# Kernel tuning notes

Measured on AMD Instinct MI355X. Metric: run time of the kernel, lower is better.

## Reference

```python
import jax, jax.numpy as jnp
import numpy as np

B, L, SD, PD, H, HD, OH = 2, 256, 64, 32, 4, 16, 32
EXP = 64  # MBConv hidden = pair_dim * expand_ratio(2)
SE = 16   # squeezed channels = int(64 * 0.25)


def _ln(x, g, b, eps=1e-5):
    m = jnp.mean(x, -1, keepdims=True)
    v = jnp.mean((x - m) ** 2, -1, keepdims=True)
    return (x - m) / jnp.sqrt(v + eps) * g + b


def _inorm(x, eps=1e-5):  # InstanceNorm2d (no affine), x: [B,C,H,W]
    m = jnp.mean(x, (2, 3), keepdims=True)
    v = jnp.mean((x - m) ** 2, (2, 3), keepdims=True)
    return (x - m) / jnp.sqrt(v + eps)


def setup_inputs() -> dict:
    key = jax.random.key(0)
    ks = jax.random.split(key, 16)
    s = jnp.float32(0.02)
    return dict(
        seq_repr=jax.random.normal(ks[0], (B, L, SD), jnp.float32),
        pair_repr=jax.random.normal(ks[1], (B, L, L, PD), jnp.float32),
        g_attn=jnp.ones((SD,), jnp.float32), b_attn=jnp.zeros((SD,), jnp.float32),
        g_pair=jnp.ones((PD,), jnp.float32), b_pair=jnp.zeros((PD,), jnp.float32),
        W_opm_lin=jax.random.normal(ks[2], (SD, OH), jnp.float32) * s,
        b_opm_lin=jnp.zeros((OH,), jnp.float32),
        g_opm=jnp.ones((OH * OH,), jnp.float32), b_opm=jnp.zeros((OH * OH,), jnp.float32),
        W_opm_proj=jax.random.normal(ks[3], (OH * OH, PD), jnp.float32) * s,
        b_opm_proj=jnp.zeros((PD,), jnp.float32),
        W_exp=jax.random.normal(ks[4], (EXP, PD), jnp.float32) * s,
        W_dw=jax.random.normal(ks[5], (EXP, 1, 3, 3), jnp.float32) * s,
        W_se1=jax.random.normal(ks[6], (SE, EXP), jnp.float32) * s,
        b_se1=jnp.zeros((SE,), jnp.float32),
        W_se2=jax.random.normal(ks[7], (EXP, SE), jnp.float32) * s,
        b_se2=jnp.zeros((EXP,), jnp.float32),
        W_pw=jax.random.normal(ks[8], (PD, EXP), jnp.float32) * s,
        W_qkv=jax.random.normal(ks[9], (SD, 3 * SD), jnp.float32) * s,
        W_outp=jax.random.normal(ks[10], (SD, SD), jnp.float32) * s,
        b_outp=jnp.zeros((SD,), jnp.float32),
        W_bias=jax.random.normal(ks[11], (PD, H), jnp.float32) * s,
    )


def reference(seq_repr, pair_repr, g_attn, b_attn, g_pair, b_pair,
              W_opm_lin, b_opm_lin, g_opm, b_opm, W_opm_proj, b_opm_proj,
              W_exp, W_dw, W_se1, b_se1, W_se2, b_se2, W_pw,
              W_qkv, W_outp, b_outp, W_bias):
    # --- OuterProductMean on attn_norm(seq) ---
    x = _ln(seq_repr, g_attn, b_attn)                            # [B,L,SD]
    a = x @ W_opm_lin + b_opm_lin                                # [B,L,OH]
    outer = jnp.einsum('bid,bje->bijde', a, a).reshape(B, L, L, OH * OH)
    op = _ln(outer, g_opm, b_opm) @ W_opm_proj + b_opm_proj      # [B,L,L,PD]
    pair = pair_repr + op
    # --- MBConv pair processor on pair_norm(pair) ---
    pn = _ln(pair, g_pair, b_pair)
    z0 = jnp.transpose(pn, (0, 3, 1, 2))                         # NCHW [B,PD,L,L]
    h = jax.nn.silu(_inorm(jnp.einsum('bcij,oc->boij', z0, W_exp)))
    h = jax.lax.conv_general_dilated(h, W_dw, (1, 1), 'SAME',
                                     feature_group_count=EXP,
                                     dimension_numbers=('NCHW', 'OIHW', 'NCHW'))
    h = jax.nn.silu(_inorm(h))
    sq = jnp.mean(h, (2, 3), keepdims=True)                      # squeeze [B,EXP,1,1]
    sq = jax.nn.silu(jnp.einsum('bcij,oc->boij', sq, W_se1) + b_se1[None, :, None, None])
    sq = jax.nn.sigmoid(jnp.einsum('bcij,oc->boij', sq, W_se2) + b_se2[None, :, None, None])
    h = h * sq
    h = _inorm(jnp.einsum('bcij,oc->boij', h, W_pw))             # project back to PD
    pair = pair + jnp.transpose(z0 + h, (0, 2, 3, 1))            # MBConv residual + outer residual
    # --- Pairwise-bias attention ---
    pn2 = _ln(pair, g_pair, b_pair)
    bias = jnp.einsum('bijp,ph->bhij', pn2, W_bias)              # [B,H,L,L]
    q, k, v = jnp.split(x @ W_qkv, 3, axis=-1)
    q = q.reshape(B, L, H, HD).transpose(0, 2, 1, 3)
    k = k.reshape(B, L, H, HD).transpose(0, 2, 1, 3)
    v = v.reshape(B, L, H, HD).transpose(0, 2, 1, 3)
    scores = jnp.einsum('bhid,bhjd->bhij', q, k) / jnp.sqrt(jnp.float32(HD)) + bias
    w = jax.nn.softmax(scores, axis=-1)
    ctx = jnp.einsum('bhij,bhjd->bhid', w, v).transpose(0, 2, 1, 3).reshape(B, L, SD)
    seq = seq_repr + ctx @ W_outp + b_outp
    return seq, pair
```

## Files before the change

### kernel.cpp

```cpp
#include <hip/hip_runtime.h>
#include <hip/hip_bf16.h>

#define LLSZ 65536
#define INV_LL (1.f / 65536.f)


__global__ __launch_bounds__(1024) void k0_prep(
    const float* __restrict__ g_opm, const float* __restrict__ b_opm,
    const float* __restrict__ Wproj, const float* __restrict__ b_proj,
    float* __restrict__ G, float* __restrict__ GW, float* __restrict__ BW)
{
    int tid = threadIdx.x;
    int p = tid & 31, rg = tid >> 5;
    float gw = 0.f, bw = 0.f;
    #pragma unroll 4
    for (int k = 0; k < 32; ++k) {
        int de = k * 32 + rg;
        float g = g_opm[de], b = b_opm[de];
        float wv = Wproj[de * 32 + p];
        float gv = g * wv;
        G[de * 32 + p] = gv;
        gw += gv;
        bw += b * wv;
    }
    __shared__ float rG[1024], rB[1024];
    rG[rg * 32 + p] = gw;
    rB[rg * 32 + p] = bw;
    __syncthreads();
    for (int s = 16; s > 0; s >>= 1) {
        if (rg < s) {
            rG[rg * 32 + p] += rG[(rg + s) * 32 + p];
            rB[rg * 32 + p] += rB[(rg + s) * 32 + p];
        }
        __syncthreads();
    }
    if (tid < 32) {
        GW[p] = rG[p];
        BW[p] = rB[p] + b_proj[p];
    }
}

__global__ __launch_bounds__(256) void k1_seq(
    const float* __restrict__ seq, const float* __restrict__ g_attn,
    const float* __restrict__ b_attn, const float* __restrict__ W_lin,
    const float* __restrict__ b_lin, const float* __restrict__ W_qkv,
    float* __restrict__ a, float* __restrict__ am, float* __restrict__ s2,
    float* __restrict__ qkv)
{
    __shared__ float Wq[64 * 192];
    __shared__ float Wl[64 * 32];
    __shared__ float xL[4][64];
    int tid = threadIdx.x;
    #pragma unroll
    for (int k = 0; k < 48; ++k) Wq[k * 256 + tid] = W_qkv[k * 256 + tid];
    #pragma unroll
    for (int k = 0; k < 8; ++k) Wl[k * 256 + tid] = W_lin[k * 256 + tid];

    int sub = tid >> 6, t = tid & 63;
    int row = blockIdx.x * 4 + sub;
    float v = seq[row * 64 + t];
    float m = v;
    for (int k = 32; k > 0; k >>= 1) m += __shfl_xor(m, k, 64);
    m *= (1.f / 64.f);
    float d = v - m;
    float var = d * d;
    for (int k = 32; k > 0; k >>= 1) var += __shfl_xor(var, k, 64);
    var *= (1.f / 64.f);
    float x = d * rsqrtf(var + 1e-5f) * g_attn[t] + b_attn[t];
    xL[sub][t] = x;
    __syncthreads();

    if (t < 32) {
        float s = 0.f;
        #pragma unroll
        for (int dd = 0; dd < 64; ++dd) s += xL[sub][dd] * Wl[dd * 32 + t];
        s += b_lin[t];
        a[row * 32 + t] = s;
        float mm = s, ss = s * s;
        for (int k = 16; k > 0; k >>= 1) {
            mm += __shfl_xor(mm, k, 32);
            ss += __shfl_xor(ss, k, 32);
        }
        if (t == 0) { am[row] = mm * (1.f / 32.f); s2[row] = ss * (1.f / 32.f); }
    }
    #pragma unroll
    for (int c3 = 0; c3 < 3; ++c3) {
        int c = c3 * 64 + t;
        float s = 0.f;
        #pragma unroll
        for (int dd = 0; dd < 64; ++dd) s += xL[sub][dd] * Wq[dd * 192 + c];
        qkv[row * 192 + c] = s;
    }
}

__global__ __launch_bounds__(256) void k2_T(
    const float* __restrict__ a, const float* __restrict__ G, float* __restrict__ T)
{
    int row = blockIdx.x;
    int tid = threadIdx.x;
    __shared__ float aL[32];
    if (tid < 32) aL[tid] = a[row * 32 + tid];
    __syncthreads();
    for (int k = 0; k < 4; ++k) {
        int idx = k * 256 + tid;
        float s = 0.f;
        #pragma unroll
        for (int d = 0; d < 32; ++d) s += aL[d] * G[d * 1024 + idx];
        T[row * 1024 + idx] = s;
    }
}

__global__ __launch_bounds__(256) void k3_op(
    const float* __restrict__ a, const float* __restrict__ am,
    const float* __restrict__ s2, const float* __restrict__ T,
    const float* __restrict__ GW, const float* __restrict__ BW,
    const float* __restrict__ pair_in, const float* __restrict__ g_pair,
    const float* __restrict__ b_pair, float* __restrict__ pair1,
    float* __restrict__ pn)
{
    int row = blockIdx.x;
    int b = row >> 8;
    int tid = threadIdx.x;
    __shared__ float Tl[1024];
    __shared__ float aL[256];
    for (int k = 0; k < 4; ++k) Tl[k * 256 + tid] = T[(long)row * 1024 + k * 256 + tid];
    float am_i = am[row], s2_i = s2[row];
    int jj = tid >> 5, p = tid & 31;
    float gw = GW[p], bw = BW[p], gp = g_pair[p], bp = b_pair[p];
    for (int jt = 0; jt < 32; ++jt) {
        __syncthreads();
        aL[tid] = a[(b * 256 + jt * 8) * 32 + tid];
        __syncthreads();
        int j = jt * 8 + jj;
        float am_j = am[b * 256 + j], s2_j = s2[b * 256 + j];
        float S = 0.f;
        #pragma unroll
        for (int e = 0; e < 32; ++e) S += aL[jj * 32 + e] * Tl[e * 32 + p];
        float m = am_i * am_j;
        float var = s2_i * s2_j - m * m;
        float isd = rsqrtf(var + 1e-5f);
        float op = isd * (S - m * gw) + bw;
        long idx = (long)row * 8192 + jt * 256 + tid;
        float pv = pair_in[idx] + op;
        pair1[idx] = pv;
        float mu = pv;
        for (int k = 16; k > 0; k >>= 1) mu += __shfl_xor(mu, k, 32);
        mu *= (1.f / 32.f);
        float dd = pv - mu;
        float vv = dd * dd;
        for (int k = 16; k > 0; k >>= 1) vv += __shfl_xor(vv, k, 32);
        vv *= (1.f / 32.f);
        pn[idx] = dd * rsqrtf(vv + 1e-5f) * gp + bp;
    }
}

__global__ __launch_bounds__(256) void k4_expand(
    const float* __restrict__ pn, const float* __restrict__ W_exp,
    float* __restrict__ e1)
{
    int blk = blockIdx.x;
    int b = blk >> 8;
    int pixbase = (blk & 255) * 256;
    int tid = threadIdx.x;
    __shared__ float pnL[256 * 33];
    __shared__ float We[64 * 32];
    for (int k = 0; k < 32; ++k) {
        int idx = k * 256 + tid;
        float v = pn[(long)b * LLSZ * 32 + (long)pixbase * 32 + idx];
        int pix = idx >> 5, c = idx & 31;
        pnL[pix * 33 + c] = v;
    }
    for (int k = 0; k < 8; ++k) We[k * 256 + tid] = W_exp[k * 256 + tid];
    __syncthreads();
    for (int o = 0; o < 64; ++o) {
        float s = 0.f;
        #pragma unroll
        for (int c = 0; c < 32; ++c) s += pnL[tid * 33 + c] * We[o * 32 + c];
        e1[(long)(b * 64 + o) * LLSZ + pixbase + tid] = s;
    }
}

__global__ __launch_bounds__(256) void k_stats(
    const float* __restrict__ buf, float* __restrict__ sum, float* __restrict__ sumsq)
{
    int bid = blockIdx.x;
    int chan = bid >> 3, seg = bid & 7;
    int tid = threadIdx.x;
    const float4* p = (const float4*)(buf + (long)chan * LLSZ + seg * 8192);
    float s = 0.f, ss = 0.f;
    #pragma unroll
    for (int k = 0; k < 8; ++k) {
        float4 v = p[k * 256 + tid];
        s += v.x + v.y + v.z + v.w;
        ss += v.x * v.x + v.y * v.y + v.z * v.z + v.w * v.w;
    }
    for (int k = 32; k > 0; k >>= 1) { s += __shfl_xor(s, k, 64); ss += __shfl_xor(ss, k, 64); }
    __shared__ float rs[4], rq[4];
    int wave = tid >> 6;
    if ((tid & 63) == 0) { rs[wave] = s; rq[wave] = ss; }
    __syncthreads();
    if (tid == 0) {
        atomicAdd(&sum[chan], rs[0] + rs[1] + rs[2] + rs[3]);
        atomicAdd(&sumsq[chan], rq[0] + rq[1] + rq[2] + rq[3]);
    }
}

__device__ __forceinline__ void chan_stats(const float* sum, const float* sumsq,
                                           int chan, float& m, float& isd)
{
    m = sum[chan] * INV_LL;
    float var = sumsq[chan] * INV_LL - m * m;
    isd = rsqrtf(var + 1e-5f);
}

__global__ __launch_bounds__(256) void k6_dw(
    const float* __restrict__ e1, const float* __restrict__ st1s,
    const float* __restrict__ st1q, const float* __restrict__ W_dw,
    float* __restrict__ h2)
{
    int blk = blockIdx.x;
    int chan = blk >> 6;
    int tile = blk & 63;
    int i0 = (tile >> 3) * 32, j0 = (tile & 7) * 32;
    int o = chan & 63;
    int tid = threadIdx.x;
    float m, isd;
    chan_stats(st1s, st1q, chan, m, isd);
    __shared__ float hT[34 * 34];
    const float* src = e1 + (long)chan * LLSZ;
    for (int idx = tid; idx < 1156; idx += 256) {
        int li = idx / 34, lj = idx % 34;
        int gi = i0 + li - 1, gj = j0 + lj - 1;
        float v = 0.f;
        if (gi >= 0 && gi < 256 && gj >= 0 && gj < 256) {
            float t = (src[gi * 256 + gj] - m) * isd;
            v = t / (1.f + expf(-t));
        }
        hT[idx] = v;
    }
    float w[9];
    #pragma unroll
    for (int k = 0; k < 9; ++k) w[k] = W_dw[o * 9 + k];
    __syncthreads();
    for (int q = 0; q < 4; ++q) {
        int pix = q * 256 + tid;
        int li = pix >> 5, lj = pix & 31;
        float s = 0.f;
        #pragma unroll
        for (int ki = 0; ki < 3; ++ki)
            #pragma unroll
            for (int kj = 0; kj < 3; ++kj)
                s += hT[(li + ki) * 34 + lj + kj] * w[ki * 3 + kj];
        h2[(long)chan * LLSZ + (i0 + li) * 256 + j0 + lj] = s;
    }
}

__global__ __launch_bounds__(256) void k8_squeeze(
    const float* __restrict__ h2, const float* __restrict__ st2s,
    const float* __restrict__ st2q, float* __restrict__ sqs)
{
    int bid = blockIdx.x;
    int chan = bid >> 3, seg = bid & 7;
    int tid = threadIdx.x;
    float m, isd;
    chan_stats(st2s, st2q, chan, m, isd);
    const float4* p = (const float4*)(h2 + (long)chan * LLSZ + seg * 8192);
    float s = 0.f;
    #pragma unroll
    for (int k = 0; k < 8; ++k) {
        float4 v = p[k * 256 + tid];
        float t;
        t = (v.x - m) * isd; s += t / (1.f + expf(-t));
        t = (v.y - m) * isd; s += t / (1.f + expf(-t));
        t = (v.z - m) * isd; s += t / (1.f + expf(-t));
        t = (v.w - m) * isd; s += t / (1.f + expf(-t));
    }
    for (int k = 32; k > 0; k >>= 1) s += __shfl_xor(s, k, 64);
    __shared__ float rs[4];
    int wave = tid >> 6;
    if ((tid & 63) == 0) rs[wave] = s;
    __syncthreads();
    if (tid == 0) atomicAdd(&sqs[chan], rs[0] + rs[1] + rs[2] + rs[3]);
}

__global__ __launch_bounds__(128) void k9_se(
    const float* __restrict__ sqs, const float* __restrict__ W1,
    const float* __restrict__ b1, const float* __restrict__ W2,
    const float* __restrict__ b2, float* __restrict__ sqv)
{
    __shared__ float s1[2 * 16];
    int tid = threadIdx.x;
    if (tid < 32) {
        int b = tid >> 4, o = tid & 15;
        float s = 0.f;
        for (int c = 0; c < 64; ++c) s += sqs[b * 64 + c] * W1[o * 64 + c];
        s = s * INV_LL + b1[o];
        s1[b * 16 + o] = s / (1.f + expf(-s));
    }
    __syncthreads();
    int b = tid >> 6, c = tid & 63;
    float s = 0.f;
    #pragma unroll
    for (int j = 0; j < 16; ++j) s += s1[b * 16 + j] * W2[c * 16 + j];
    s += b2[c];
    sqv[b * 64 + c] = 1.f / (1.f + expf(-s));
}

__global__ __launch_bounds__(256) void k10_pw(
    const float* __restrict__ h2, const float* __restrict__ st2s,
    const float* __restrict__ st2q, const float* __restrict__ sqv,
    const float* __restrict__ W_pw, float* __restrict__ hp)
{
    int blk = blockIdx.x;
    int b = blk >> 8;
    int pixbase = (blk & 255) * 256;
    int tid = threadIdx.x;
    __shared__ float hL[32 * 256];
    __shared__ float Wp[32 * 64];
    for (int k = 0; k < 8; ++k) Wp[k * 256 + tid] = W_pw[k * 256 + tid];
    float acc[32];
    #pragma unroll
    for (int p = 0; p < 32; ++p) acc[p] = 0.f;
    for (int half = 0; half < 2; ++half) {
        __syncthreads();
        for (int c = 0; c < 32; ++c) {
            int chan = b * 64 + half * 32 + c;
            float m, isd;
            chan_stats(st2s, st2q, chan, m, isd);
            float v = h2[(long)chan * LLSZ + pixbase + tid];
            float t = (v - m) * isd;
            hL[c * 256 + tid] = (t / (1.f + expf(-t))) * sqv[chan];
        }
        __syncthreads();
        #pragma unroll
        for (int p = 0; p < 32; ++p) {
            float s = 0.f;
            #pragma unroll
            for (int c = 0; c < 32; ++c) s += hL[c * 256 + tid] * Wp[p * 64 + half * 32 + c];
            acc[p] += s;
        }
    }
    for (int p = 0; p < 32; ++p)
        hp[(long)(b * 32 + p) * LLSZ + pixbase + tid] = acc[p];
}

__global__ __launch_bounds__(256) void k12_merge(
    const float* __restrict__ pair1, const float* __restrict__ pn,
    const float* __restrict__ hp, const float* __restrict__ st3s,
    const float* __restrict__ st3q, const float* __restrict__ g_pair,
    const float* __restrict__ b_pair, const float* __restrict__ W_bias,
    float* __restrict__ pair_out, float* __restrict__ biasbuf)
{
    int blk = blockIdx.x;
    int b = blk >> 8;
    int pixbase = (blk & 255) * 256;
    int tid = threadIdx.x;
    __shared__ float hpL[32 * 257];
    for (int p = 0; p < 32; ++p) {
        int chan = b * 32 + p;
        float m, isd;
        chan_stats(st3s, st3q, chan, m, isd);
        float v = hp[(long)chan * LLSZ + pixbase + tid];
        hpL[p * 257 + tid] = (v - m) * isd;
    }
    __syncthreads();
    int jj = tid >> 5, p = tid & 31;
    float gp = g_pair[p], bp = b_pair[p];
    float wb0 = W_bias[p * 4 + 0], wb1 = W_bias[p * 4 + 1];
    float wb2 = W_bias[p * 4 + 2], wb3 = W_bias[p * 4 + 3];
    for (int it = 0; it < 32; ++it) {
        int pix = it * 8 + jj;
        long idx = (long)b * LLSZ * 32 + (long)(pixbase + pix) * 32 + p;
        float v = pair1[idx] + pn[idx] + hpL[p * 257 + pix];
        pair_out[idx] = v;
        float mu = v;
        for (int k = 16; k > 0; k >>= 1) mu += __shfl_xor(mu, k, 32);
        mu *= (1.f / 32.f);
        float d = v - mu;
        float vv = d * d;
        for (int k = 16; k > 0; k >>= 1) vv += __shfl_xor(vv, k, 32);
        vv *= (1.f / 32.f);
        float pn2 = d * rsqrtf(vv + 1e-5f) * gp + bp;
        float t0 = pn2 * wb0, t1 = pn2 * wb1, t2 = pn2 * wb2, t3 = pn2 * wb3;
        for (int k = 16; k > 0; k >>= 1) {
            t0 += __shfl_xor(t0, k, 32);
            t1 += __shfl_xor(t1, k, 32);
            t2 += __shfl_xor(t2, k, 32);
            t3 += __shfl_xor(t3, k, 32);
        }
        if (p == 0) {
            int ij = pixbase + pix;
            biasbuf[(long)(b * 4 + 0) * LLSZ + ij] = t0;
            biasbuf[(long)(b * 4 + 1) * LLSZ + ij] = t1;
            biasbuf[(long)(b * 4 + 2) * LLSZ + ij] = t2;
            biasbuf[(long)(b * 4 + 3) * LLSZ + ij] = t3;
        }
    }
}

__global__ __launch_bounds__(256) void k13_attn(
    const float* __restrict__ qkv, const float* __restrict__ biasbuf,
    float* __restrict__ ctx)
{
    int blk = blockIdx.x;
    int i = blk & 255;
    int h = (blk >> 8) & 3;
    int b = blk >> 10;
    int tid = threadIdx.x;
    __shared__ float qL[16];
    __shared__ float red[256];
    __shared__ float wL[256];
    __shared__ float pL[256];
    if (tid < 16) qL[tid] = qkv[(long)(b * 256 + i) * 192 + h * 16 + tid];
    __syncthreads();
    const float* krow = qkv + (long)(b * 256 + tid) * 192 + 64 + h * 16;
    float s = 0.f;
    #pragma unroll
    for (int d = 0; d < 16; ++d) s += qL[d] * krow[d];
    s = s * 0.25f + biasbuf[(long)(b * 4 + h) * LLSZ + i * 256 + tid];
    red[tid] = s;
    __syncthreads();
    for (int k = 128; k > 0; k >>= 1) {
        if (tid < k) red[tid] = fmaxf(red[tid], red[tid + k]);
        __syncthreads();
    }
    float mx = red[0];
    __syncthreads();
    float w = expf(s - mx);
    wL[tid] = w;
    red[tid] = w;
    __syncthreads();
    for (int k = 128; k > 0; k >>= 1) {
        if (tid < k) red[tid] += red[tid + k];
        __syncthreads();
    }
    float inv = 1.f / red[0];
    int d = tid & 15, jg = tid >> 4;
    const float* vbase = qkv + 128 + h * 16 + d;
    float ps = 0.f;
    #pragma unroll
    for (int jjj = 0; jjj < 16; ++jjj) {
        int jn = jg * 16 + jjj;
        ps += wL[jn] * vbase[(long)(b * 256 + jn) * 192];
    }
    pL[tid] = ps;
    __syncthreads();
    if (tid < 16) {
        float c = 0.f;
        #pragma unroll
        for (int jg2 = 0; jg2 < 16; ++jg2) c += pL[jg2 * 16 + tid];
        ctx[(long)(b * 256 + i) * 64 + h * 16 + tid] = c * inv;
    }
}

__global__ __launch_bounds__(256) void k14_seqout(
    const float* __restrict__ seq, const float* __restrict__ ctx,
    const float* __restrict__ W_outp, const float* __restrict__ b_outp,
    float* __restrict__ out)
{
    __shared__ float Wo[64 * 64];
    __shared__ float cL[4][64];
    int tid = threadIdx.x;
    #pragma unroll
    for (int k = 0; k < 16; ++k) Wo[k * 256 + tid] = W_outp[k * 256 + tid];
    int sub = tid >> 6, t = tid & 63;
    int row = blockIdx.x * 4 + sub;
    cL[sub][t] = ctx[row * 64 + t];
    __syncthreads();
    float s = b_outp[t];
    #pragma unroll
    for (int u = 0; u < 64; ++u) s += cL[sub][u] * Wo[u * 64 + t];
    out[row * 64 + t] = seq[row * 64 + t] + s;
}

extern "C" void kernel_launch(void* const* d_in, const int* in_sizes, int n_in,
                              void* d_out, int out_size, void* d_ws, size_t ws_size,
                              hipStream_t stream) {
    const float* seq_repr   = (const float*)d_in[0];
    const float* pair_repr  = (const float*)d_in[1];
    const float* g_attn     = (const float*)d_in[2];
    const float* b_attn     = (const float*)d_in[3];
    const float* g_pair     = (const float*)d_in[4];
    const float* b_pair     = (const float*)d_in[5];
    const float* W_opm_lin  = (const float*)d_in[6];
    const float* b_opm_lin  = (const float*)d_in[7];
    const float* g_opm      = (const float*)d_in[8];
    const float* b_opm      = (const float*)d_in[9];
    const float* W_opm_proj = (const float*)d_in[10];
    const float* b_opm_proj = (const float*)d_in[11];
    const float* W_exp      = (const float*)d_in[12];
    const float* W_dw       = (const float*)d_in[13];
    const float* W_se1      = (const float*)d_in[14];
    const float* b_se1      = (const float*)d_in[15];
    const float* W_se2      = (const float*)d_in[16];
    const float* b_se2      = (const float*)d_in[17];
    const float* W_pw       = (const float*)d_in[18];
    const float* W_qkv      = (const float*)d_in[19];
    const float* W_outp     = (const float*)d_in[20];
    const float* b_outp     = (const float*)d_in[21];
    const float* W_bias     = (const float*)d_in[22];

    float* out_seq  = (float*)d_out;
    float* out_pair = (float*)d_out + 32768;

    float* w = (float*)d_ws;
    float* a_buf   = w;
    float* am_buf  = a_buf + 16384;
    float* s2_buf  = am_buf + 512;
    float* qkv_buf = s2_buf + 512;
    float* G_buf   = qkv_buf + 98304;
    float* GW_buf  = G_buf + 32768;
    float* BW_buf  = GW_buf + 32;
    float* ctx     = BW_buf + 32;
    float* st1s    = ctx + 32768;
    float* st1q    = st1s + 128;
    float* st2s    = st1q + 128;
    float* st2q    = st2s + 128;
    float* st3s    = st2q + 128;
    float* st3q    = st3s + 64;
    float* sqs     = st3q + 64;
    float* sqv     = sqs + 128;
    float* T_buf   = sqv + 128;
    float* biasb   = T_buf;
    float* pair1   = T_buf + 524288;
    float* pn      = pair1 + 4194304;
    float* e1      = pn + 4194304;
    float* hp      = e1;
    float* h2      = e1 + 8388608;

    hipMemsetAsync(st1s, 0, 768 * sizeof(float), stream);

    hipLaunchKernelGGL(k0_prep, dim3(1), dim3(1024), 0, stream,
                       g_opm, b_opm, W_opm_proj, b_opm_proj, G_buf, GW_buf, BW_buf);
    hipLaunchKernelGGL(k1_seq, dim3(128), dim3(256), 0, stream,
                       seq_repr, g_attn, b_attn, W_opm_lin, b_opm_lin, W_qkv,
                       a_buf, am_buf, s2_buf, qkv_buf);
    hipLaunchKernelGGL(k2_T, dim3(512), dim3(256), 0, stream, a_buf, G_buf, T_buf);
    hipLaunchKernelGGL(k3_op, dim3(512), dim3(256), 0, stream,
                       a_buf, am_buf, s2_buf, T_buf, GW_buf, BW_buf,
                       pair_repr, g_pair, b_pair, pair1, pn);
    hipLaunchKernelGGL(k4_expand, dim3(512), dim3(256), 0, stream, pn, W_exp, e1);
    hipLaunchKernelGGL(k_stats, dim3(1024), dim3(256), 0, stream, e1, st1s, st1q);
    hipLaunchKernelGGL(k6_dw, dim3(8192), dim3(256), 0, stream, e1, st1s, st1q, W_dw, h2);
    hipLaunchKernelGGL(k_stats, dim3(1024), dim3(256), 0, stream, h2, st2s, st2q);
    hipLaunchKernelGGL(k8_squeeze, dim3(1024), dim3(256), 0, stream, h2, st2s, st2q, sqs);
    hipLaunchKernelGGL(k9_se, dim3(1), dim3(128), 0, stream,
                       sqs, W_se1, b_se1, W_se2, b_se2, sqv);
    hipLaunchKernelGGL(k10_pw, dim3(512), dim3(256), 0, stream,
                       h2, st2s, st2q, sqv, W_pw, hp);
    hipLaunchKernelGGL(k_stats, dim3(512), dim3(256), 0, stream, hp, st3s, st3q);
    hipLaunchKernelGGL(k12_merge, dim3(512), dim3(256), 0, stream,
                       pair1, pn, hp, st3s, st3q, g_pair, b_pair, W_bias,
                       out_pair, biasb);
    hipLaunchKernelGGL(k13_attn, dim3(2048), dim3(256), 0, stream, qkv_buf, biasb, ctx);
    hipLaunchKernelGGL(k14_seqout, dim3(128), dim3(256), 0, stream,
                       seq_repr, ctx, W_outp, b_outp, out_seq);
}
```

Measured before the change: 329.2 us.

## Fuse LayerNorm recompute, SE and stats into neighbors; vectorize and retile kernels

```diff
diff --git a/kernel.cpp b/kernel.cpp
--- a/kernel.cpp
+++ b/kernel.cpp
@@ -4,6 +4,16 @@
 #define LLSZ 65536
 #define INV_LL (1.f / 65536.f)
 
+
+__device__ __forceinline__ void chan_stats(const float* sum, const float* sumsq,
+                                           int chan, float& m, float& isd)
+{
+    m = sum[chan] * INV_LL;
+    float var = sumsq[chan] * INV_LL - m * m;
+    isd = rsqrtf(var + 1e-5f);
+}
+
+__device__ __forceinline__ float silu(float t) { return t / (1.f + expf(-t)); }
 
 __global__ __launch_bounds__(1024) void k0_prep(
     const float* __restrict__ g_opm, const float* __restrict__ b_opm,
@@ -16,12 +26,11 @@
     #pragma unroll 4
     for (int k = 0; k < 32; ++k) {
         int de = k * 32 + rg;
-        float g = g_opm[de], b = b_opm[de];
         float wv = Wproj[de * 32 + p];
-        float gv = g * wv;
+        float gv = g_opm[de] * wv;
         G[de * 32 + p] = gv;
         gw += gv;
-        bw += b * wv;
+        bw += b_opm[de] * wv;
     }
     __shared__ float rG[1024], rB[1024];
     rG[rg * 32 + p] = gw;
@@ -34,10 +43,7 @@
         }
         __syncthreads();
     }
-    if (tid < 32) {
-        GW[p] = rG[p];
-        BW[p] = rB[p] + b_proj[p];
-    }
+    if (tid < 32) { GW[p] = rG[p]; BW[p] = rB[p] + b_proj[p]; }
 }
 
 __global__ __launch_bounds__(256) void k1_seq(
@@ -114,69 +120,88 @@
     const float* __restrict__ a, const float* __restrict__ am,
     const float* __restrict__ s2, const float* __restrict__ T,
     const float* __restrict__ GW, const float* __restrict__ BW,
-    const float* __restrict__ pair_in, const float* __restrict__ g_pair,
-    const float* __restrict__ b_pair, float* __restrict__ pair1,
-    float* __restrict__ pn)
-{
-    int row = blockIdx.x;
+    const float* __restrict__ pair_in, float* __restrict__ pair1)
+{
+    int blk = blockIdx.x;
+    int row = blk >> 3;
+    int jg = blk & 7;
     int b = row >> 8;
+    int j0 = jg * 32;
     int tid = threadIdx.x;
     __shared__ float Tl[1024];
-    __shared__ float aL[256];
-    for (int k = 0; k < 4; ++k) Tl[k * 256 + tid] = T[(long)row * 1024 + k * 256 + tid];
+    __shared__ float aL[32 * 33];
+    __shared__ float amL[32], s2L[32], gwL[32], bwL[32];
+    ((float4*)Tl)[tid] = ((const float4*)(T + (long)row * 1024))[tid];
+    for (int k = 0; k < 4; ++k) {
+        int idx = k * 256 + tid;
+        aL[(idx >> 5) * 33 + (idx & 31)] = a[(b * 256 + j0) * 32 + idx];
+    }
+    if (tid < 32) {
+        amL[tid] = am[b * 256 + j0 + tid];
+        s2L[tid] = s2[b * 256 + j0 + tid];
+        gwL[tid] = GW[tid];
+        bwL[tid] = BW[tid];
+    }
+    __syncthreads();
+    int jl = tid >> 3, cq = tid & 7;
     float am_i = am[row], s2_i = s2[row];
-    int jj = tid >> 5, p = tid & 31;
-    float gw = GW[p], bw = BW[p], gp = g_pair[p], bp = b_pair[p];
-    for (int jt = 0; jt < 32; ++jt) {
-        __syncthreads();
-        aL[tid] = a[(b * 256 + jt * 8) * 32 + tid];
-        __syncthreads();
-        int j = jt * 8 + jj;
-        float am_j = am[b * 256 + j], s2_j = s2[b * 256 + j];
+    float m = am_i * amL[jl];
+    float isd = rsqrtf(s2_i * s2L[jl] - m * m + 1e-5f);
+    long base = ((long)row * 256 + j0 + jl) * 32 + cq * 4;
+    float4 pv = *(const float4*)(pair_in + base);
+    float o[4];
+    #pragma unroll
+    for (int u = 0; u < 4; ++u) {
+        int p = cq * 4 + u;
         float S = 0.f;
         #pragma unroll
-        for (int e = 0; e < 32; ++e) S += aL[jj * 32 + e] * Tl[e * 32 + p];
-        float m = am_i * am_j;
-        float var = s2_i * s2_j - m * m;
-        float isd = rsqrtf(var + 1e-5f);
-        float op = isd * (S - m * gw) + bw;
-        long idx = (long)row * 8192 + jt * 256 + tid;
-        float pv = pair_in[idx] + op;
-        pair1[idx] = pv;
-        float mu = pv;
-        for (int k = 16; k > 0; k >>= 1) mu += __shfl_xor(mu, k, 32);
-        mu *= (1.f / 32.f);
-        float dd = pv - mu;
-        float vv = dd * dd;
-        for (int k = 16; k > 0; k >>= 1) vv += __shfl_xor(vv, k, 32);
-        vv *= (1.f / 32.f);
-        pn[idx] = dd * rsqrtf(vv + 1e-5f) * gp + bp;
-    }
+        for (int e = 0; e < 32; ++e) S += aL[jl * 33 + e] * Tl[e * 32 + p];
+        o[u] = isd * (S - m * gwL[p]) + bwL[p];
+    }
+    pv.x += o[0]; pv.y += o[1]; pv.z += o[2]; pv.w += o[3];
+    *(float4*)(pair1 + base) = pv;
 }
 
 __global__ __launch_bounds__(256) void k4_expand(
-    const float* __restrict__ pn, const float* __restrict__ W_exp,
+    const float* __restrict__ pair1, const float* __restrict__ g_pair,
+    const float* __restrict__ b_pair, const float* __restrict__ W_exp,
     float* __restrict__ e1)
 {
     int blk = blockIdx.x;
-    int b = blk >> 8;
-    int pixbase = (blk & 255) * 256;
-    int tid = threadIdx.x;
-    __shared__ float pnL[256 * 33];
-    __shared__ float We[64 * 32];
-    for (int k = 0; k < 32; ++k) {
+    int b = blk >> 9;
+    int pixbase = (blk & 511) * 128;
+    int tid = threadIdx.x;
+    __shared__ float pnL[128 * 33];
+    __shared__ float We[2048];
+    __shared__ float gL[32], bL[32];
+    for (int k = 0; k < 8; ++k) We[k * 256 + tid] = W_exp[k * 256 + tid];
+    if (tid < 32) { gL[tid] = g_pair[tid]; bL[tid] = b_pair[tid]; }
+    const float4* src = (const float4*)(pair1 + ((long)b * LLSZ + pixbase) * 32);
+    for (int k = 0; k < 4; ++k) {
         int idx = k * 256 + tid;
-        float v = pn[(long)b * LLSZ * 32 + (long)pixbase * 32 + idx];
-        int pix = idx >> 5, c = idx & 31;
-        pnL[pix * 33 + c] = v;
-    }
-    for (int k = 0; k < 8; ++k) We[k * 256 + tid] = W_exp[k * 256 + tid];
-    __syncthreads();
-    for (int o = 0; o < 64; ++o) {
-        float s = 0.f;
-        #pragma unroll
-        for (int c = 0; c < 32; ++c) s += pnL[tid * 33 + c] * We[o * 32 + c];
-        e1[(long)(b * 64 + o) * LLSZ + pixbase + tid] = s;
+        int pix = idx >> 3, cq = idx & 7;
+        float4 v = src[idx];
+        pnL[pix * 33 + cq * 4 + 0] = v.x;
+        pnL[pix * 33 + cq * 4 + 1] = v.y;
+        pnL[pix * 33 + cq * 4 + 2] = v.z;
+        pnL[pix * 33 + cq * 4 + 3] = v.w;
+    }
+    __syncthreads();
+    int pix = tid & 127, og = tid >> 7;
+    float s = 0.f, q = 0.f;
+    #pragma unroll
+    for (int c = 0; c < 32; ++c) { float v = pnL[pix * 33 + c]; s += v; q += v * v; }
+    float mu = s * (1.f / 32.f);
+    float isd = rsqrtf(q * (1.f / 32.f) - mu * mu + 1e-5f);
+    float x[32];
+    #pragma unroll
+    for (int c = 0; c < 32; ++c) x[c] = (pnL[pix * 33 + c] - mu) * isd * gL[c] + bL[c];
+    for (int oo = 0; oo < 32; ++oo) {
+        int o = og * 32 + oo;
+        float acc = 0.f;
+        #pragma unroll
+        for (int c = 0; c < 32; ++c) acc += x[c] * We[o * 32 + c];
+        e1[((long)(b * 64 + o)) * LLSZ + pixbase + pix] = acc;
     }
 }
 
@@ -205,53 +230,50 @@
     }
 }
 
-__device__ __forceinline__ void chan_stats(const float* sum, const float* sumsq,
-                                           int chan, float& m, float& isd)
-{
-    m = sum[chan] * INV_LL;
-    float var = sumsq[chan] * INV_LL - m * m;
-    isd = rsqrtf(var + 1e-5f);
-}
-
 __global__ __launch_bounds__(256) void k6_dw(
     const float* __restrict__ e1, const float* __restrict__ st1s,
     const float* __restrict__ st1q, const float* __restrict__ W_dw,
     float* __restrict__ h2)
 {
     int blk = blockIdx.x;
-    int chan = blk >> 6;
-    int tile = blk & 63;
-    int i0 = (tile >> 3) * 32, j0 = (tile & 7) * 32;
+    int chan = blk >> 5;
+    int r0 = (blk & 31) * 8;
     int o = chan & 63;
     int tid = threadIdx.x;
     float m, isd;
     chan_stats(st1s, st1q, chan, m, isd);
-    __shared__ float hT[34 * 34];
+    __shared__ float sL[10][258];
     const float* src = e1 + (long)chan * LLSZ;
-    for (int idx = tid; idx < 1156; idx += 256) {
-        int li = idx / 34, lj = idx % 34;
-        int gi = i0 + li - 1, gj = j0 + lj - 1;
-        float v = 0.f;
-        if (gi >= 0 && gi < 256 && gj >= 0 && gj < 256) {
-            float t = (src[gi * 256 + gj] - m) * isd;
-            v = t / (1.f + expf(-t));
-        }
-        hT[idx] = v;
-    }
+    for (int k = tid; k < 640; k += 256) {
+        int rr = k >> 6, c4 = k & 63;
+        int g = r0 - 1 + rr;
+        float4 v = make_float4(0.f, 0.f, 0.f, 0.f);
+        if (g >= 0 && g < 256) v = *(const float4*)(src + g * 256 + c4 * 4);
+        float t;
+        t = (v.x - m) * isd; v.x = (g >= 0 && g < 256) ? silu(t) : 0.f;
+        t = (v.y - m) * isd; v.y = (g >= 0 && g < 256) ? silu(t) : 0.f;
+        t = (v.z - m) * isd; v.z = (g >= 0 && g < 256) ? silu(t) : 0.f;
+        t = (v.w - m) * isd; v.w = (g >= 0 && g < 256) ? silu(t) : 0.f;
+        sL[rr][1 + c4 * 4 + 0] = v.x;
+        sL[rr][1 + c4 * 4 + 1] = v.y;
+        sL[rr][1 + c4 * 4 + 2] = v.z;
+        sL[rr][1 + c4 * 4 + 3] = v.w;
+    }
+    if (tid < 10) { sL[tid][0] = 0.f; sL[tid][257] = 0.f; }
     float w[9];
     #pragma unroll
     for (int k = 0; k < 9; ++k) w[k] = W_dw[o * 9 + k];
     __syncthreads();
-    for (int q = 0; q < 4; ++q) {
-        int pix = q * 256 + tid;
-        int li = pix >> 5, lj = pix & 31;
+    int c = tid;
+    #pragma unroll
+    for (int rr = 0; rr < 8; ++rr) {
         float s = 0.f;
         #pragma unroll
         for (int ki = 0; ki < 3; ++ki)
             #pragma unroll
             for (int kj = 0; kj < 3; ++kj)
-                s += hT[(li + ki) * 34 + lj + kj] * w[ki * 3 + kj];
-        h2[(long)chan * LLSZ + (i0 + li) * 256 + j0 + lj] = s;
+                s += sL[rr + ki][c + kj] * w[ki * 3 + kj];
+        h2[(long)chan * LLSZ + (r0 + rr) * 256 + c] = s;
     }
 }
 
@@ -269,11 +291,8 @@
     #pragma unroll
     for (int k = 0; k < 8; ++k) {
         float4 v = p[k * 256 + tid];
-        float t;
-        t = (v.x - m) * isd; s += t / (1.f + expf(-t));
-        t = (v.y - m) * isd; s += t / (1.f + expf(-t));
-        t = (v.z - m) * isd; s += t / (1.f + expf(-t));
-        t = (v.w - m) * isd; s += t / (1.f + expf(-t));
+        s += silu((v.x - m) * isd) + silu((v.y - m) * isd)
+           + silu((v.z - m) * isd) + silu((v.w - m) * isd);
     }
     for (int k = 32; k > 0; k >>= 1) s += __shfl_xor(s, k, 64);
     __shared__ float rs[4];
@@ -283,53 +302,56 @@
     if (tid == 0) atomicAdd(&sqs[chan], rs[0] + rs[1] + rs[2] + rs[3]);
 }
 
-__global__ __launch_bounds__(128) void k9_se(
-    const float* __restrict__ sqs, const float* __restrict__ W1,
-    const float* __restrict__ b1, const float* __restrict__ W2,
-    const float* __restrict__ b2, float* __restrict__ sqv)
-{
-    __shared__ float s1[2 * 16];
-    int tid = threadIdx.x;
-    if (tid < 32) {
-        int b = tid >> 4, o = tid & 15;
-        float s = 0.f;
-        for (int c = 0; c < 64; ++c) s += sqs[b * 64 + c] * W1[o * 64 + c];
-        s = s * INV_LL + b1[o];
-        s1[b * 16 + o] = s / (1.f + expf(-s));
-    }
-    __syncthreads();
-    int b = tid >> 6, c = tid & 63;
-    float s = 0.f;
-    #pragma unroll
-    for (int j = 0; j < 16; ++j) s += s1[b * 16 + j] * W2[c * 16 + j];
-    s += b2[c];
-    sqv[b * 64 + c] = 1.f / (1.f + expf(-s));
-}
-
 __global__ __launch_bounds__(256) void k10_pw(
     const float* __restrict__ h2, const float* __restrict__ st2s,
-    const float* __restrict__ st2q, const float* __restrict__ sqv,
-    const float* __restrict__ W_pw, float* __restrict__ hp)
+    const float* __restrict__ st2q, const float* __restrict__ sqs,
+    const float* __restrict__ W_se1, const float* __restrict__ b_se1,
+    const float* __restrict__ W_se2, const float* __restrict__ b_se2,
+    const float* __restrict__ W_pw, float* __restrict__ hp,
+    float* __restrict__ st3s, float* __restrict__ st3q)
 {
     int blk = blockIdx.x;
     int b = blk >> 8;
     int pixbase = (blk & 255) * 256;
     int tid = threadIdx.x;
     __shared__ float hL[32 * 256];
-    __shared__ float Wp[32 * 64];
+    __shared__ float Wp[2048];
+    __shared__ float s1L[16];
+    __shared__ float sqvL[64];
+    __shared__ float red[4][32], redq[4][32];
     for (int k = 0; k < 8; ++k) Wp[k * 256 + tid] = W_pw[k * 256 + tid];
+    if (tid < 16) {
+        float s = 0.f;
+        for (int c = 0; c < 64; ++c) s += sqs[b * 64 + c] * W_se1[tid * 64 + c];
+        s = s * INV_LL + b_se1[tid];
+        s1L[tid] = silu(s);
+    }
+    __syncthreads();
+    if (tid < 64) {
+        float s = 0.f;
+        #pragma unroll
+        for (int j = 0; j < 16; ++j) s += s1L[j] * W_se2[tid * 16 + j];
+        s += b_se2[tid];
+        sqvL[tid] = 1.f / (1.f + expf(-s));
+    }
     float acc[32];
     #pragma unroll
     for (int p = 0; p < 32; ++p) acc[p] = 0.f;
     for (int half = 0; half < 2; ++half) {
         __syncthreads();
-        for (int c = 0; c < 32; ++c) {
+        for (int k = 0; k < 8; ++k) {
+            int idx = k * 256 + tid;
+            int c = idx >> 6, q4 = idx & 63;
             int chan = b * 64 + half * 32 + c;
             float m, isd;
             chan_stats(st2s, st2q, chan, m, isd);
-            float v = h2[(long)chan * LLSZ + pixbase + tid];
-            float t = (v - m) * isd;
-            hL[c * 256 + tid] = (t / (1.f + expf(-t))) * sqv[chan];
+            float sc = sqvL[half * 32 + c];
+            float4 v = *(const float4*)(h2 + (long)chan * LLSZ + pixbase + q4 * 4);
+            v.x = silu((v.x - m) * isd) * sc;
+            v.y = silu((v.y - m) * isd) * sc;
+            v.z = silu((v.z - m) * isd) * sc;
+            v.w = silu((v.w - m) * isd) * sc;
+            *(float4*)(hL + c * 256 + q4 * 4) = v;
         }
         __syncthreads();
         #pragma unroll
@@ -340,60 +362,99 @@
             acc[p] += s;
         }
     }
-    for (int p = 0; p < 32; ++p)
-        hp[(long)(b * 32 + p) * LLSZ + pixbase + tid] = acc[p];
+    int wave = tid >> 6, lane = tid & 63;
+    #pragma unroll
+    for (int p = 0; p < 32; ++p) {
+        float v = acc[p];
+        hp[((long)(b * 32 + p)) * LLSZ + pixbase + tid] = v;
+        float s = v, q = v * v;
+        for (int k = 32; k > 0; k >>= 1) { s += __shfl_xor(s, k, 64); q += __shfl_xor(q, k, 64); }
+        if (lane == 0) { red[wave][p] = s; redq[wave][p] = q; }
+    }
+    __syncthreads();
+    if (tid < 32) {
+        atomicAdd(&st3s[b * 32 + tid], red[0][tid] + red[1][tid] + red[2][tid] + red[3][tid]);
+        atomicAdd(&st3q[b * 32 + tid], redq[0][tid] + redq[1][tid] + redq[2][tid] + redq[3][tid]);
+    }
 }
 
 __global__ __launch_bounds__(256) void k12_merge(
-    const float* __restrict__ pair1, const float* __restrict__ pn,
-    const float* __restrict__ hp, const float* __restrict__ st3s,
-    const float* __restrict__ st3q, const float* __restrict__ g_pair,
-    const float* __restrict__ b_pair, const float* __restrict__ W_bias,
-    float* __restrict__ pair_out, float* __restrict__ biasbuf)
+    const float* __restrict__ pair1, const float* __restrict__ hp,
+    const float* __restrict__ st3s, const float* __restrict__ st3q,
+    const float* __restrict__ g_pair, const float* __restrict__ b_pair,
+    const float* __restrict__ W_bias, float* __restrict__ pair_out,
+    float* __restrict__ biasbuf)
 {
     int blk = blockIdx.x;
     int b = blk >> 8;
     int pixbase = (blk & 255) * 256;
     int tid = threadIdx.x;
-    __shared__ float hpL[32 * 257];
-    for (int p = 0; p < 32; ++p) {
+    __shared__ float hpL[32][257];
+    for (int k = 0; k < 8; ++k) {
+        int idx = k * 256 + tid;
+        int p = idx >> 6, q4 = idx & 63;
         int chan = b * 32 + p;
         float m, isd;
         chan_stats(st3s, st3q, chan, m, isd);
-        float v = hp[(long)chan * LLSZ + pixbase + tid];
-        hpL[p * 257 + tid] = (v - m) * isd;
-    }
-    __syncthreads();
-    int jj = tid >> 5, p = tid & 31;
-    float gp = g_pair[p], bp = b_pair[p];
-    float wb0 = W_bias[p * 4 + 0], wb1 = W_bias[p * 4 + 1];
-    float wb2 = W_bias[p * 4 + 2], wb3 = W_bias[p * 4 + 3];
-    for (int it = 0; it < 32; ++it) {
-        int pix = it * 8 + jj;
-        long idx = (long)b * LLSZ * 32 + (long)(pixbase + pix) * 32 + p;
-        float v = pair1[idx] + pn[idx] + hpL[p * 257 + pix];
-        pair_out[idx] = v;
-        float mu = v;
-        for (int k = 16; k > 0; k >>= 1) mu += __shfl_xor(mu, k, 32);
-        mu *= (1.f / 32.f);
-        float d = v - mu;
-        float vv = d * d;
-        for (int k = 16; k > 0; k >>= 1) vv += __shfl_xor(vv, k, 32);
-        vv *= (1.f / 32.f);
-        float pn2 = d * rsqrtf(vv + 1e-5f) * gp + bp;
-        float t0 = pn2 * wb0, t1 = pn2 * wb1, t2 = pn2 * wb2, t3 = pn2 * wb3;
-        for (int k = 16; k > 0; k >>= 1) {
-            t0 += __shfl_xor(t0, k, 32);
-            t1 += __shfl_xor(t1, k, 32);
-            t2 += __shfl_xor(t2, k, 32);
-            t3 += __shfl_xor(t3, k, 32);
-        }
-        if (p == 0) {
-            int ij = pixbase + pix;
-            biasbuf[(long)(b * 4 + 0) * LLSZ + ij] = t0;
-            biasbuf[(long)(b * 4 + 1) * LLSZ + ij] = t1;
-            biasbuf[(long)(b * 4 + 2) * LLSZ + ij] = t2;
-            biasbuf[(long)(b * 4 + 3) * LLSZ + ij] = t3;
+        float4 v = *(const float4*)(hp + (long)chan * LLSZ + pixbase + q4 * 4);
+        hpL[p][q4 * 4 + 0] = (v.x - m) * isd;
+        hpL[p][q4 * 4 + 1] = (v.y - m) * isd;
+        hpL[p][q4 * 4 + 2] = (v.z - m) * isd;
+        hpL[p][q4 * 4 + 3] = (v.w - m) * isd;
+    }
+    __syncthreads();
+    int pg = tid >> 3, cq = tid & 7;
+    float gp[4], bp[4], wb[4][4];
+    #pragma unroll
+    for (int u = 0; u < 4; ++u) {
+        int c = cq * 4 + u;
+        gp[u] = g_pair[c]; bp[u] = b_pair[c];
+        #pragma unroll
+        for (int h = 0; h < 4; ++h) wb[u][h] = W_bias[c * 4 + h];
+    }
+    for (int it = 0; it < 8; ++it) {
+        int pix = it * 32 + pg;
+        long base = ((long)b * LLSZ + pixbase + pix) * 32;
+        float4 v1 = *(const float4*)(pair1 + base + cq * 4);
+        float s = v1.x + v1.y + v1.z + v1.w;
+        float q = v1.x * v1.x + v1.y * v1.y + v1.z * v1.z + v1.w * v1.w;
+        s += __shfl_xor(s, 1, 8); q += __shfl_xor(q, 1, 8);
+        s += __shfl_xor(s, 2, 8); q += __shfl_xor(q, 2, 8);
+        s += __shfl_xor(s, 4, 8); q += __shfl_xor(q, 4, 8);
+        float mu = s * (1.f / 32.f);
+        float isd = rsqrtf(q * (1.f / 32.f) - mu * mu + 1e-5f);
+        float vo[4], vv1[4] = {v1.x, v1.y, v1.z, v1.w};
+        #pragma unroll
+        for (int u = 0; u < 4; ++u) {
+            float pnv = (vv1[u] - mu) * isd * gp[u] + bp[u];
+            vo[u] = vv1[u] + pnv + hpL[cq * 4 + u][pix];
+        }
+        float4 vout = make_float4(vo[0], vo[1], vo[2], vo[3]);
+        *(float4*)(pair_out + base + cq * 4) = vout;
+        float s2_ = vo[0] + vo[1] + vo[2] + vo[3];
+        float q2 = vo[0] * vo[0] + vo[1] * vo[1] + vo[2] * vo[2] + vo[3] * vo[3];
+        s2_ += __shfl_xor(s2_, 1, 8); q2 += __shfl_xor(q2, 1, 8);
+        s2_ += __shfl_xor(s2_, 2, 8); q2 += __shfl_xor(q2, 2, 8);
+        s2_ += __shfl_xor(s2_, 4, 8); q2 += __shfl_xor(q2, 4, 8);
+        float mu2 = s2_ * (1.f / 32.f);
+        float isd2 = rsqrtf(q2 * (1.f / 32.f) - mu2 * mu2 + 1e-5f);
+        float t[4] = {0.f, 0.f, 0.f, 0.f};
+        #pragma unroll
+        for (int u = 0; u < 4; ++u) {
+            float pn2 = (vo[u] - mu2) * isd2 * gp[u] + bp[u];
+            #pragma unroll
+            for (int h = 0; h < 4; ++h) t[h] += pn2 * wb[u][h];
+        }
+        #pragma unroll
+        for (int h = 0; h < 4; ++h) {
+            t[h] += __shfl_xor(t[h], 1, 8);
+            t[h] += __shfl_xor(t[h], 2, 8);
+            t[h] += __shfl_xor(t[h], 4, 8);
+        }
+        if (cq == 0) {
+            #pragma unroll
+            for (int h = 0; h < 4; ++h)
+                biasbuf[((long)(b * 4 + h)) * LLSZ + pixbase + pix] = t[h];
         }
     }
 }
@@ -403,53 +464,48 @@
     float* __restrict__ ctx)
 {
     int blk = blockIdx.x;
-    int i = blk & 255;
-    int h = (blk >> 8) & 3;
-    int b = blk >> 10;
-    int tid = threadIdx.x;
-    __shared__ float qL[16];
-    __shared__ float red[256];
-    __shared__ float wL[256];
-    __shared__ float pL[256];
-    if (tid < 16) qL[tid] = qkv[(long)(b * 256 + i) * 192 + h * 16 + tid];
-    __syncthreads();
-    const float* krow = qkv + (long)(b * 256 + tid) * 192 + 64 + h * 16;
-    float s = 0.f;
-    #pragma unroll
-    for (int d = 0; d < 16; ++d) s += qL[d] * krow[d];
-    s = s * 0.25f + biasbuf[(long)(b * 4 + h) * LLSZ + i * 256 + tid];
-    red[tid] = s;
-    __syncthreads();
-    for (int k = 128; k > 0; k >>= 1) {
-        if (tid < k) red[tid] = fmaxf(red[tid], red[tid + k]);
-        __syncthreads();
-    }
-    float mx = red[0];
-    __syncthreads();
-    float w = expf(s - mx);
-    wL[tid] = w;
-    red[tid] = w;
-    __syncthreads();
-    for (int k = 128; k > 0; k >>= 1) {
-        if (tid < k) red[tid] += red[tid + k];
-        __syncthreads();
-    }
-    float inv = 1.f / red[0];
-    int d = tid & 15, jg = tid >> 4;
-    const float* vbase = qkv + 128 + h * 16 + d;
-    float ps = 0.f;
-    #pragma unroll
-    for (int jjj = 0; jjj < 16; ++jjj) {
-        int jn = jg * 16 + jjj;
-        ps += wL[jn] * vbase[(long)(b * 256 + jn) * 192];
-    }
-    pL[tid] = ps;
-    __syncthreads();
-    if (tid < 16) {
-        float c = 0.f;
-        #pragma unroll
-        for (int jg2 = 0; jg2 < 16; ++jg2) c += pL[jg2 * 16 + tid];
-        ctx[(long)(b * 256 + i) * 64 + h * 16 + tid] = c * inv;
+    int b = blk >> 8;
+    int h = (blk >> 6) & 3;
+    int ig = blk & 63;
+    int wave = threadIdx.x >> 6, lane = threadIdx.x & 63;
+    int i = ig * 4 + wave;
+    const float* qrow = qkv + ((long)(b * 256 + i)) * 192 + h * 16;
+    float qv[16];
+    #pragma unroll
+    for (int d = 0; d < 16; ++d) qv[d] = qrow[d];
+    float sj[4];
+    #pragma unroll
+    for (int q = 0; q < 4; ++q) {
+        int j = lane + 64 * q;
+        const float* kr = qkv + ((long)(b * 256 + j)) * 192 + 64 + h * 16;
+        float s = 0.f;
+        #pragma unroll
+        for (int d = 0; d < 16; ++d) s += qv[d] * kr[d];
+        sj[q] = s * 0.25f + biasbuf[((long)(b * 4 + h)) * LLSZ + i * 256 + j];
+    }
+    float mx = fmaxf(fmaxf(sj[0], sj[1]), fmaxf(sj[2], sj[3]));
+    for (int k = 32; k > 0; k >>= 1) mx = fmaxf(mx, __shfl_xor(mx, k, 64));
+    float wgt[4], wsum = 0.f;
+    #pragma unroll
+    for (int q = 0; q < 4; ++q) { wgt[q] = expf(sj[q] - mx); wsum += wgt[q]; }
+    for (int k = 32; k > 0; k >>= 1) wsum += __shfl_xor(wsum, k, 64);
+    float inv = 1.f / wsum;
+    float o[16];
+    #pragma unroll
+    for (int d = 0; d < 16; ++d) o[d] = 0.f;
+    #pragma unroll
+    for (int q = 0; q < 4; ++q) {
+        const float* vr = qkv + ((long)(b * 256 + lane + 64 * q)) * 192 + 128 + h * 16;
+        #pragma unroll
+        for (int d = 0; d < 16; ++d) o[d] += wgt[q] * vr[d];
+    }
+    #pragma unroll
+    for (int d = 0; d < 16; ++d)
+        for (int k = 32; k > 0; k >>= 1) o[d] += __shfl_xor(o[d], k, 64);
+    if (lane == 0) {
+        #pragma unroll
+        for (int d = 0; d < 16; ++d)
+            ctx[((long)(b * 256 + i)) * 64 + h * 16 + d] = o[d] * inv;
     }
 }
 
@@ -519,12 +575,10 @@
     float* st3s    = st2q + 128;
     float* st3q    = st3s + 64;
     float* sqs     = st3q + 64;
-    float* sqv     = sqs + 128;
-    float* T_buf   = sqv + 128;
+    float* T_buf   = sqs + 128;
     float* biasb   = T_buf;
     float* pair1   = T_buf + 524288;
-    float* pn      = pair1 + 4194304;
-    float* e1      = pn + 4194304;
+    float* e1      = pair1 + 4194304;
     float* hp      = e1;
     float* h2      = e1 + 8388608;
 
@@ -536,23 +590,25 @@
                        seq_repr, g_attn, b_attn, W_opm_lin, b_opm_lin, W_qkv,
                        a_buf, am_buf, s2_buf, qkv_buf);
     hipLaunchKernelGGL(k2_T, dim3(512), dim3(256), 0, stream, a_buf, G_buf, T_buf);
-    hipLaunchKernelGGL(k3_op, dim3(512), dim3(256), 0, stream,
+    hipLaunchKernelGGL(k3_op, dim3(4096), dim3(256), 0, stream,
                        a_buf, am_buf, s2_buf, T_buf, GW_buf, BW_buf,
-                       pair_repr, g_pair, b_pair, pair1, pn);
-    hipLaunchKernelGGL(k4_expand, dim3(512), dim3(256), 0, stream, pn, W_exp, e1);
+                       pair_repr, pair1);
+    hipLaunchKernelGGL(k4_expand, dim3(1024), dim3(256), 0, stream,
+                       pair1, g_pair, b_pair, W_exp, e1);
     hipLaunchKernelGGL(k_stats, dim3(1024), dim3(256), 0, stream, e1, st1s, st1q);
-    hipLaunchKernelGGL(k6_dw, dim3(8192), dim3(256), 0, stream, e1, st1s, st1q, W_dw, h2);
+    hipLaunchKernelGGL(k6_dw, dim3(4096), dim3(256), 0, stream,
+                       e1, st1s, st1q, W_dw, h2);
     hipLaunchKernelGGL(k_stats, dim3(1024), dim3(256), 0, stream, h2, st2s, st2q);
-    hipLaunchKernelGGL(k8_squeeze, dim3(1024), dim3(256), 0, stream, h2, st2s, st2q, sqs);
-    hipLaunchKernelGGL(k9_se, dim3(1), dim3(128), 0, stream,
-                       sqs, W_se1, b_se1, W_se2, b_se2, sqv);
+    hipLaunchKernelGGL(k8_squeeze, dim3(1024), dim3(256), 0, stream,
+                       h2, st2s, st2q, sqs);
     hipLaunchKernelGGL(k10_pw, dim3(512), dim3(256), 0, stream,
-                       h2, st2s, st2q, sqv, W_pw, hp);
-    hipLaunchKernelGGL(k_stats, dim3(512), dim3(256), 0, stream, hp, st3s, st3q);
+                       h2, st2s, st2q, sqs, W_se1, b_se1, W_se2, b_se2,
+                       W_pw, hp, st3s, st3q);
     hipLaunchKernelGGL(k12_merge, dim3(512), dim3(256), 0, stream,
-                       pair1, pn, hp, st3s, st3q, g_pair, b_pair, W_bias,
+                       pair1, hp, st3s, st3q, g_pair, b_pair, W_bias,
                        out_pair, biasb);
-    hipLaunchKernelGGL(k13_attn, dim3(2048), dim3(256), 0, stream, qkv_buf, biasb, ctx);
+    hipLaunchKernelGGL(k13_attn, dim3(512), dim3(256), 0, stream,
+                       qkv_buf, biasb, ctx);
     hipLaunchKernelGGL(k14_seqout, dim3(128), dim3(256), 0, stream,
                        seq_repr, ctx, W_outp, b_outp, out_seq);
 }
```

After: 282.7 us. 1.16x faster.
